# Performance work log

Measured on AMD Instinct MI355X. Metric: run time of the kernel, lower is better.

Reference implementation:

```python
import jax, jax.numpy as jnp
import numpy as np

B, S, E, H, F = 8, 1024, 1024, 16, 4096
D = E // H  # head_dim = 64
EPS = 1e-5


def setup_inputs() -> dict:
    key = jax.random.key(0)
    ks = jax.random.split(key, 12)
    s = 0.02
    return {
        "x": jax.random.normal(ks[0], (B, S, E), dtype=jnp.float32),
        # per-head projections (shared across heads), torch stores [out,in]; we use [in,out]
        "Wq": jax.random.normal(ks[1], (D, D), dtype=jnp.float32) * s,
        "Wk": jax.random.normal(ks[2], (D, D), dtype=jnp.float32) * s,
        "Wv": jax.random.normal(ks[3], (D, D), dtype=jnp.float32) * s,
        "Wo": jax.random.normal(ks[4], (E, E), dtype=jnp.float32) * s,
        "bo": jnp.zeros((E,), dtype=jnp.float32),
        "W1": jax.random.normal(ks[5], (E, F), dtype=jnp.float32) * s,
        "b1": jnp.zeros((F,), dtype=jnp.float32),
        "W2": jax.random.normal(ks[6], (F, E), dtype=jnp.float32) * s,
        "b2": jnp.zeros((E,), dtype=jnp.float32),
        "g1": jnp.ones((E,), dtype=jnp.float32),
        "beta1": jnp.zeros((E,), dtype=jnp.float32),
        "g2": jnp.ones((E,), dtype=jnp.float32),
        "beta2": jnp.zeros((E,), dtype=jnp.float32),
    }


def _layer_norm(x, g, b):
    m = jnp.mean(x, axis=-1, keepdims=True)
    v = jnp.mean(jnp.square(x - m), axis=-1, keepdims=True)
    return (x - m) * jax.lax.rsqrt(v + EPS) * g + b


def reference(x, Wq, Wk, Wv, Wo, bo, W1, b1, W2, b2, g1, beta1, g2, beta2):
    b, s, e = x.shape
    # --- attention sublayer (pre-norm) ---
    nx = _layer_norm(x, g1, beta1)
    h = nx.reshape(b, s, H, D)              # [B,S,H,D]
    q = h @ Wq                               # per-head linear, weight shared over heads
    k = h @ Wk
    v = h @ Wv
    energy = jnp.einsum('bqhd,bkhd->bhqk', q, k)  # full [B,H,S,S] scores
    mask = jnp.tril(jnp.ones((s, s), dtype=bool))
    energy = jnp.where(mask, energy, -jnp.inf)
    att = jax.nn.softmax(energy / jnp.sqrt(jnp.float32(e)), axis=-1)  # NOTE: scale by sqrt(embed_dim)
    o = jnp.einsum('bhqk,bkhd->bqhd', att, v).reshape(b, s, e)
    x = x + (o @ Wo + bo)
    # --- MLP sublayer (pre-norm); dropout is identity in eval ---
    nx = _layer_norm(x, g2, beta2)
    x = x + (jax.nn.relu(nx @ W1 + b1) @ W2 + b2)
    return x
```

## Files before the change

kernel.cpp:

```cpp
#include <hip/hip_runtime.h>

typedef unsigned short u16;
typedef __attribute__((ext_vector_type(4))) float f4;
typedef __attribute__((ext_vector_type(8))) short s8v;
typedef __attribute__((ext_vector_type(4))) unsigned short u16x4;

#define DEVINL __device__ __forceinline__

DEVINL float b2f(u16 u) { union { unsigned i; float f; } x; x.i = ((unsigned)u) << 16; return x.f; }
DEVINL u16 f2b(float f) {
  union { float f; unsigned i; } x; x.f = f;
  unsigned r = 0x7FFFu + ((x.i >> 16) & 1u);
  return (u16)((x.i + r) >> 16);
}

#define GLD_LDS16(g, l)                                                        \
  __builtin_amdgcn_global_load_lds((__attribute__((address_space(1))) void*)(g), \
                                   (__attribute__((address_space(3))) void*)(l), 16, 0, 0)

__global__ __launch_bounds__(256) void k_transpose(const float* __restrict__ in,
                                                   u16* __restrict__ out, int R, int C) {
  __shared__ float t[32][33];
  int tx = threadIdx.x & 31, ty = threadIdx.x >> 5;
  int c0 = blockIdx.x * 32, r0 = blockIdx.y * 32;
#pragma unroll
  for (int i = 0; i < 32; i += 8)
    t[ty + i][tx] = in[(long)(r0 + ty + i) * C + (c0 + tx)];
  __syncthreads();
#pragma unroll
  for (int i = 0; i < 32; i += 8)
    out[(long)(c0 + ty + i) * R + (r0 + tx)] = f2b(t[tx][ty + i]);
}

__global__ __launch_bounds__(256) void k_vtrans(const u16* __restrict__ v, u16* __restrict__ vt) {
  __shared__ u16 t[64][72];
  int bh = blockIdx.x, b = bh >> 4, h = bh & 15;
  int s0 = blockIdx.y * 64;
  int tid = threadIdx.x;
#pragma unroll
  for (int p = 0; p < 2; ++p) {
    int idx = p * 256 + tid;
    int sl = idx >> 3, c8 = (idx & 7) * 8;
    *(s8v*)(&t[sl][c8]) = *(const s8v*)(v + (((long)(b * 1024 + s0 + sl) * 16 + h) * 64) + c8);
  }
  __syncthreads();
#pragma unroll
  for (int p = 0; p < 2; ++p) {
    int idx = p * 256 + tid;
    int d = idx >> 3, c8 = (idx & 7) * 8;
    s8v o;
#pragma unroll
    for (int e = 0; e < 8; ++e) o[e] = (short)t[c8 + e][d];
    *(s8v*)(vt + ((long)bh * 64 + d) * 1024 + s0 + c8) = o;
  }
}

__global__ __launch_bounds__(256) void k_layernorm(const float* __restrict__ x,
                                                   const float* __restrict__ g,
                                                   const float* __restrict__ be,
                                                   u16* __restrict__ out) {
  long row = blockIdx.x;
  int tid = threadIdx.x;
  f4 v = ((const f4*)(x + row * 1024))[tid];
  float s = v[0] + v[1] + v[2] + v[3];
  float s2 = v[0] * v[0] + v[1] * v[1] + v[2] * v[2] + v[3] * v[3];
#pragma unroll
  for (int off = 32; off > 0; off >>= 1) {
    s += __shfl_down(s, off, 64);
    s2 += __shfl_down(s2, off, 64);
  }
  __shared__ float red[8];
  int wv = tid >> 6, ln = tid & 63;
  if (ln == 0) { red[wv] = s; red[4 + wv] = s2; }
  __syncthreads();
  s = red[0] + red[1] + red[2] + red[3];
  s2 = red[4] + red[5] + red[6] + red[7];
  float mean = s * (1.0f / 1024.0f);
  float var = s2 * (1.0f / 1024.0f) - mean * mean;
  float rs = rsqrtf(var + 1e-5f);
  f4 gg = ((const f4*)g)[tid];
  f4 bb = ((const f4*)be)[tid];
  u16x4 o;
#pragma unroll
  for (int i = 0; i < 4; ++i) o[i] = f2b((v[i] - mean) * rs * gg[i] + bb[i]);
  ((u16x4*)(out + row * 1024))[tid] = o;
}

__global__ __launch_bounds__(256) void k_qkv(const u16* __restrict__ nx, const u16* __restrict__ WqT,
                                             const u16* __restrict__ WkT, const u16* __restrict__ WvT,
                                             u16* __restrict__ q, u16* __restrict__ k,
                                             u16* __restrict__ v) {
  int tid = threadIdx.x, lane = tid & 63, wave = tid >> 6;
  int quad = lane >> 4, l16 = lane & 15;
  long rbase = (long)blockIdx.x * 64 + wave * 16;
  s8v a0 = *(const s8v*)(nx + (rbase + l16) * 64 + quad * 8);
  s8v a1 = *(const s8v*)(nx + (rbase + l16) * 64 + 32 + quad * 8);
  const u16* Ws[3] = {WqT, WkT, WvT};
  u16* Os[3] = {q, k, v};
#pragma unroll
  for (int t = 0; t < 3; ++t) {
#pragma unroll
    for (int j = 0; j < 4; ++j) {
      s8v b0 = *(const s8v*)(Ws[t] + (j * 16 + l16) * 64 + quad * 8);
      s8v b1 = *(const s8v*)(Ws[t] + (j * 16 + l16) * 64 + 32 + quad * 8);
      f4 acc = {0.f, 0.f, 0.f, 0.f};
      acc = __builtin_amdgcn_mfma_f32_16x16x32_bf16(a0, b0, acc, 0, 0, 0);
      acc = __builtin_amdgcn_mfma_f32_16x16x32_bf16(a1, b1, acc, 0, 0, 0);
#pragma unroll
      for (int r = 0; r < 4; ++r)
        Os[t][(rbase + quad * 4 + r) * 64 + j * 16 + l16] = f2b(acc[r]);
    }
  }
}

__global__ __launch_bounds__(256) void k_attn_mfma(const u16* __restrict__ q,
                                                   const u16* __restrict__ kk,
                                                   const u16* __restrict__ vt,
                                                   u16* __restrict__ o) {
  constexpr int LDK = 72;
  __shared__ u16 Ks[64 * LDK];
  __shared__ u16 Vt[64 * LDK];
  __shared__ u16 Ps[4][16 * LDK];
  int tid = threadIdx.x, lane = tid & 63, wave = tid >> 6;
  int quad = lane >> 4, l16 = lane & 15;
  int b = blockIdx.x >> 4, h = blockIdx.x & 15;
  int qi = (int)gridDim.y - 1 - (int)blockIdx.y;
  int q0 = qi * 64 + wave * 16;

  const u16* qp = q + (((long)(b * 1024 + q0 + l16)) * 16 + h) * 64;
  s8v aq0 = *(const s8v*)(qp + quad * 8);
  s8v aq1 = *(const s8v*)(qp + 32 + quad * 8);

  f4 O[4];
  float m_[4], l_[4];
#pragma unroll
  for (int jd = 0; jd < 4; ++jd) O[jd] = f4{0.f, 0.f, 0.f, 0.f};
#pragma unroll
  for (int r = 0; r < 4; ++r) { m_[r] = -__builtin_inff(); l_[r] = 0.f; }

  for (int kt = 0; kt <= qi; ++kt) {
    __syncthreads();
#pragma unroll
    for (int p = 0; p < 2; ++p) {
      int idx = p * 256 + tid;
      int row = idx >> 3, c8 = (idx & 7) * 8;
      *(s8v*)(Ks + row * LDK + c8) =
          *(const s8v*)(kk + (((long)(b * 1024 + kt * 64 + row)) * 16 + h) * 64 + c8);
      *(s8v*)(Vt + row * LDK + c8) =
          *(const s8v*)(vt + ((long)blockIdx.x * 64 + row) * 1024 + kt * 64 + c8);
    }
    __syncthreads();

    f4 sf[4];
#pragma unroll
    for (int jn = 0; jn < 4; ++jn) {
      s8v b0 = *(const s8v*)(Ks + (jn * 16 + l16) * LDK + quad * 8);
      s8v b1 = *(const s8v*)(Ks + (jn * 16 + l16) * LDK + 32 + quad * 8);
      f4 acc = f4{0.f, 0.f, 0.f, 0.f};
      acc = __builtin_amdgcn_mfma_f32_16x16x32_bf16(aq0, b0, acc, 0, 0, 0);
      acc = __builtin_amdgcn_mfma_f32_16x16x32_bf16(aq1, b1, acc, 0, 0, 0);
      sf[jn] = acc;
    }
    bool diag = (kt == qi);
    float rm[4];
#pragma unroll
    for (int r = 0; r < 4; ++r) rm[r] = -__builtin_inff();
#pragma unroll
    for (int jn = 0; jn < 4; ++jn)
#pragma unroll
      for (int r = 0; r < 4; ++r) {
        float v = sf[jn][r] * 0.03125f;
        if (diag && (jn * 16 + l16 > wave * 16 + quad * 4 + r)) v = -__builtin_inff();
        sf[jn][r] = v;
        rm[r] = fmaxf(rm[r], v);
      }
#pragma unroll
    for (int off = 1; off < 16; off <<= 1)
#pragma unroll
      for (int r = 0; r < 4; ++r) rm[r] = fmaxf(rm[r], __shfl_xor(rm[r], off, 64));
    float alpha[4], rs[4];
#pragma unroll
    for (int r = 0; r < 4; ++r) {
      float mn = fmaxf(m_[r], rm[r]);
      alpha[r] = __expf(m_[r] - mn);
      m_[r] = mn;
      rs[r] = 0.f;
    }
#pragma unroll
    for (int jn = 0; jn < 4; ++jn)
#pragma unroll
      for (int r = 0; r < 4; ++r) {
        float p = __expf(sf[jn][r] - m_[r]);
        rs[r] += p;
        Ps[wave][(quad * 4 + r) * LDK + jn * 16 + l16] = f2b(p);
      }
#pragma unroll
    for (int off = 1; off < 16; off <<= 1)
#pragma unroll
      for (int r = 0; r < 4; ++r) rs[r] += __shfl_xor(rs[r], off, 64);
#pragma unroll
    for (int r = 0; r < 4; ++r) l_[r] = l_[r] * alpha[r] + rs[r];
#pragma unroll
    for (int jd = 0; jd < 4; ++jd)
#pragma unroll
      for (int r = 0; r < 4; ++r) O[jd][r] *= alpha[r];
    asm volatile("s_waitcnt lgkmcnt(0)" ::: "memory");
    s8v p0 = *(const s8v*)(&Ps[wave][l16 * LDK + quad * 8]);
    s8v p1 = *(const s8v*)(&Ps[wave][l16 * LDK + 32 + quad * 8]);
#pragma unroll
    for (int jd = 0; jd < 4; ++jd) {
      s8v b0 = *(const s8v*)(Vt + (jd * 16 + l16) * LDK + quad * 8);
      s8v b1 = *(const s8v*)(Vt + (jd * 16 + l16) * LDK + 32 + quad * 8);
      O[jd] = __builtin_amdgcn_mfma_f32_16x16x32_bf16(p0, b0, O[jd], 0, 0, 0);
      O[jd] = __builtin_amdgcn_mfma_f32_16x16x32_bf16(p1, b1, O[jd], 0, 0, 0);
    }
  }
#pragma unroll
  for (int r = 0; r < 4; ++r) {
    float inv = 1.0f / l_[r];
    u16* op = o + (((long)(b * 1024 + q0 + quad * 4 + r)) * 16 + h) * 64;
#pragma unroll
    for (int jd = 0; jd < 4; ++jd) op[jd * 16 + l16] = f2b(O[jd][r] * inv);
  }
}

template <int EPI>
__global__ __launch_bounds__(256) void k_gemm_bt(const u16* __restrict__ A, const u16* __restrict__ BT,
                                                 const float* __restrict__ bias,
                                                 const float* __restrict__ resid,
                                                 void* __restrict__ outp, int M, int N, int K) {
  __shared__ u16 sA[3][128 * 32];
  __shared__ u16 sB[3][128 * 32];
  int tid = threadIdx.x, lane = tid & 63, wave = tid >> 6;
  int quad = lane >> 4, l16 = lane & 15;
  int wm = wave >> 1, wn = wave & 1;
  long bm = blockIdx.x, bn = blockIdx.y;
  int srow = tid >> 2, scol = (tid & 3) * 8;
  const u16* ga = A + (bm * 128 + srow) * (long)K + scol;
  const u16* gb = BT + (bn * 128 + srow) * (long)K + scol;
  int woff = wave * 1024;

  f4 acc[4][4];
#pragma unroll
  for (int i = 0; i < 4; ++i)
#pragma unroll
    for (int j = 0; j < 4; ++j) acc[i][j] = f4{0.f, 0.f, 0.f, 0.f};

#pragma unroll
  for (int t = 0; t < 2; ++t) {
    char* lA = (char*)&sA[t][0] + woff;
    char* lB = (char*)&sB[t][0] + woff;
    GLD_LDS16(ga + t * 32, lA);
    GLD_LDS16(ga + 64 * (long)K + t * 32, lA + 4096);
    GLD_LDS16(gb + t * 32, lB);
    GLD_LDS16(gb + 64 * (long)K + t * 32, lB + 4096);
  }

  int cur = 0;
  for (int k0 = 0; k0 < K; k0 += 32) {
    int k2 = k0 + 64;
    if (k2 < K) {
      asm volatile("s_waitcnt vmcnt(4)\n\ts_barrier" ::: "memory");
      int nb = cur >= 1 ? cur - 1 : 2;
      char* lA = (char*)&sA[nb][0] + woff;
      char* lB = (char*)&sB[nb][0] + woff;
      GLD_LDS16(ga + k2, lA);
      GLD_LDS16(ga + 64 * (long)K + k2, lA + 4096);
      GLD_LDS16(gb + k2, lB);
      GLD_LDS16(gb + 64 * (long)K + k2, lB + 4096);
    } else {
      asm volatile("s_waitcnt vmcnt(0)\n\ts_barrier" ::: "memory");
    }
    const u16* cA = sA[cur];
    const u16* cB = sB[cur];
    s8v aF[4], bF[4];
#pragma unroll
    for (int i = 0; i < 4; ++i)
      aF[i] = *(const s8v*)(cA + (wm * 64 + i * 16 + l16) * 32 + quad * 8);
#pragma unroll
    for (int j = 0; j < 4; ++j)
      bF[j] = *(const s8v*)(cB + (wn * 64 + j * 16 + l16) * 32 + quad * 8);
#pragma unroll
    for (int i = 0; i < 4; ++i)
#pragma unroll
      for (int j = 0; j < 4; ++j)
        acc[i][j] = __builtin_amdgcn_mfma_f32_16x16x32_bf16(aF[i], bF[j], acc[i][j], 0, 0, 0);
    cur = cur < 2 ? cur + 1 : 0;
  }

#pragma unroll
  for (int i = 0; i < 4; ++i) {
#pragma unroll
    for (int j = 0; j < 4; ++j) {
      long row = bm * 128 + wm * 64 + i * 16 + quad * 4;
      int col = (int)bn * 128 + wn * 64 + j * 16 + l16;
      float bcol = bias[col];
#pragma unroll
      for (int r = 0; r < 4; ++r) {
        float val = acc[i][j][r] + bcol;
        if (EPI == 1) {
          ((u16*)outp)[(row + r) * (long)N + col] = f2b(val > 0.f ? val : 0.f);
        } else {
          ((float*)outp)[(row + r) * (long)N + col] = resid[(row + r) * (long)N + col] + val;
        }
      }
    }
  }
}

extern "C" void kernel_launch(void* const* d_in, const int* in_sizes, int n_in, void* d_out,
                              int out_size, void* d_ws, size_t ws_size, hipStream_t stream) {
  const float* x = (const float*)d_in[0];
  const float* Wq = (const float*)d_in[1];
  const float* Wk = (const float*)d_in[2];
  const float* Wv = (const float*)d_in[3];
  const float* Wo = (const float*)d_in[4];
  const float* bo = (const float*)d_in[5];
  const float* W1 = (const float*)d_in[6];
  const float* b1 = (const float*)d_in[7];
  const float* W2 = (const float*)d_in[8];
  const float* b2 = (const float*)d_in[9];
  const float* g1 = (const float*)d_in[10];
  const float* be1 = (const float*)d_in[11];
  const float* g2 = (const float*)d_in[12];
  const float* be2 = (const float*)d_in[13];

  char* ws = (char*)d_ws;
  const size_t MB = 1ull << 20;
  u16* nx = (u16*)(ws + 0);
  u16* qb = (u16*)(ws + 16 * MB);
  u16* kb = (u16*)(ws + 32 * MB);
  u16* vb = (u16*)(ws + 48 * MB);
  float* x1 = (float*)(ws + 64 * MB);
  u16* h1 = (u16*)(ws + 96 * MB);
  u16* vtr = (u16*)(ws + 96 * MB);
  u16* WoT = (u16*)(ws + 160 * MB);
  u16* W1T = (u16*)(ws + 162 * MB);
  u16* W2T = (u16*)(ws + 170 * MB);
  u16* WqT = (u16*)(ws + 178 * MB);
  u16* WkT = WqT + 64 * 64;
  u16* WvT = WkT + 64 * 64;
  u16* ob = nx;
  u16* nx2 = qb;

  k_transpose<<<dim3(32, 32), 256, 0, stream>>>(Wo, WoT, 1024, 1024);
  k_transpose<<<dim3(128, 32), 256, 0, stream>>>(W1, W1T, 1024, 4096);
  k_transpose<<<dim3(32, 128), 256, 0, stream>>>(W2, W2T, 4096, 1024);
  k_transpose<<<dim3(2, 2), 256, 0, stream>>>(Wq, WqT, 64, 64);
  k_transpose<<<dim3(2, 2), 256, 0, stream>>>(Wk, WkT, 64, 64);
  k_transpose<<<dim3(2, 2), 256, 0, stream>>>(Wv, WvT, 64, 64);

  k_layernorm<<<8192, 256, 0, stream>>>(x, g1, be1, nx);
  k_qkv<<<2048, 256, 0, stream>>>(nx, WqT, WkT, WvT, qb, kb, vb);
  k_vtrans<<<dim3(128, 16), 256, 0, stream>>>(vb, vtr);
  k_attn_mfma<<<dim3(128, 16), 256, 0, stream>>>(qb, kb, vtr, ob);
  k_gemm_bt<2><<<dim3(64, 8), 256, 0, stream>>>(ob, WoT, bo, x, x1, 8192, 1024, 1024);

  k_layernorm<<<8192, 256, 0, stream>>>(x1, g2, be2, nx2);
  k_gemm_bt<1><<<dim3(64, 32), 256, 0, stream>>>(nx2, W1T, b1, nullptr, h1, 8192, 4096, 1024);
  k_gemm_bt<2><<<dim3(64, 8), 256, 0, stream>>>(h1, W2T, b2, x1, d_out, 8192, 1024, 4096);
}
```

Before: 457.0 us.

## Enlarge attention query tile, fold softmax scale into Q, store residual as bf16

```diff
diff --git a/kernel.cpp b/kernel.cpp
--- a/kernel.cpp
+++ b/kernel.cpp
@@ -55,13 +55,20 @@
   }
 }
 
-__global__ __launch_bounds__(256) void k_layernorm(const float* __restrict__ x,
+template <int IT>
+__global__ __launch_bounds__(256) void k_layernorm(const void* __restrict__ xv,
                                                    const float* __restrict__ g,
                                                    const float* __restrict__ be,
                                                    u16* __restrict__ out) {
   long row = blockIdx.x;
   int tid = threadIdx.x;
-  f4 v = ((const f4*)(x + row * 1024))[tid];
+  f4 v;
+  if (IT == 0) {
+    v = ((const f4*)((const float*)xv + row * 1024))[tid];
+  } else {
+    u16x4 t = ((const u16x4*)((const u16*)xv + row * 1024))[tid];
+    v = f4{b2f(t[0]), b2f(t[1]), b2f(t[2]), b2f(t[3])};
+  }
   float s = v[0] + v[1] + v[2] + v[3];
   float s2 = v[0] * v[0] + v[1] * v[1] + v[2] * v[2] + v[3] * v[3];
 #pragma unroll
@@ -99,6 +106,7 @@
   u16* Os[3] = {q, k, v};
 #pragma unroll
   for (int t = 0; t < 3; ++t) {
+    const float scale = (t == 0) ? 0.03125f : 1.0f;
 #pragma unroll
     for (int j = 0; j < 4; ++j) {
       s8v b0 = *(const s8v*)(Ws[t] + (j * 16 + l16) * 64 + quad * 8);
@@ -108,7 +116,7 @@
       acc = __builtin_amdgcn_mfma_f32_16x16x32_bf16(a1, b1, acc, 0, 0, 0);
 #pragma unroll
       for (int r = 0; r < 4; ++r)
-        Os[t][(rbase + quad * 4 + r) * 64 + j * 16 + l16] = f2b(acc[r]);
+        Os[t][(rbase + quad * 4 + r) * 64 + j * 16 + l16] = f2b(acc[r] * scale);
     }
   }
 }
@@ -120,25 +128,35 @@
   constexpr int LDK = 72;
   __shared__ u16 Ks[64 * LDK];
   __shared__ u16 Vt[64 * LDK];
-  __shared__ u16 Ps[4][16 * LDK];
+  __shared__ u16 Ps[4][32 * LDK];
   int tid = threadIdx.x, lane = tid & 63, wave = tid >> 6;
   int quad = lane >> 4, l16 = lane & 15;
   int b = blockIdx.x >> 4, h = blockIdx.x & 15;
   int qi = (int)gridDim.y - 1 - (int)blockIdx.y;
-  int q0 = qi * 64 + wave * 16;
-
-  const u16* qp = q + (((long)(b * 1024 + q0 + l16)) * 16 + h) * 64;
-  s8v aq0 = *(const s8v*)(qp + quad * 8);
-  s8v aq1 = *(const s8v*)(qp + 32 + quad * 8);
-
-  f4 O[4];
-  float m_[4], l_[4];
-#pragma unroll
-  for (int jd = 0; jd < 4; ++jd) O[jd] = f4{0.f, 0.f, 0.f, 0.f};
-#pragma unroll
-  for (int r = 0; r < 4; ++r) { m_[r] = -__builtin_inff(); l_[r] = 0.f; }
-
-  for (int kt = 0; kt <= qi; ++kt) {
+  int Q0 = qi * 128;
+  int q0 = Q0 + wave * 32;
+
+  s8v aq[2][2];
+#pragma unroll
+  for (int mt = 0; mt < 2; ++mt) {
+    const u16* qp = q + (((long)(b * 1024 + q0 + mt * 16 + l16)) * 16 + h) * 64;
+    aq[mt][0] = *(const s8v*)(qp + quad * 8);
+    aq[mt][1] = *(const s8v*)(qp + 32 + quad * 8);
+  }
+
+  f4 O[2][4];
+  float m_[2][4], l_[2][4];
+#pragma unroll
+  for (int mt = 0; mt < 2; ++mt)
+#pragma unroll
+    for (int jd = 0; jd < 4; ++jd) O[mt][jd] = f4{0.f, 0.f, 0.f, 0.f};
+#pragma unroll
+  for (int mt = 0; mt < 2; ++mt)
+#pragma unroll
+    for (int r = 0; r < 4; ++r) { m_[mt][r] = -__builtin_inff(); l_[mt][r] = 0.f; }
+
+  int ntiles = 2 * qi + 2;
+  for (int kt = 0; kt < ntiles; ++kt) {
     __syncthreads();
 #pragma unroll
     for (int p = 0; p < 2; ++p) {
@@ -151,83 +169,96 @@
     }
     __syncthreads();
 
-    f4 sf[4];
-#pragma unroll
-    for (int jn = 0; jn < 4; ++jn) {
-      s8v b0 = *(const s8v*)(Ks + (jn * 16 + l16) * LDK + quad * 8);
-      s8v b1 = *(const s8v*)(Ks + (jn * 16 + l16) * LDK + 32 + quad * 8);
-      f4 acc = f4{0.f, 0.f, 0.f, 0.f};
-      acc = __builtin_amdgcn_mfma_f32_16x16x32_bf16(aq0, b0, acc, 0, 0, 0);
-      acc = __builtin_amdgcn_mfma_f32_16x16x32_bf16(aq1, b1, acc, 0, 0, 0);
-      sf[jn] = acc;
-    }
-    bool diag = (kt == qi);
-    float rm[4];
-#pragma unroll
-    for (int r = 0; r < 4; ++r) rm[r] = -__builtin_inff();
-#pragma unroll
-    for (int jn = 0; jn < 4; ++jn)
+    bool pv[2];
+#pragma unroll
+    for (int mt = 0; mt < 2; ++mt) {
+      int base = q0 + mt * 16;
+      pv[mt] = (kt * 64 <= base + 15);
+      if (!pv[mt]) continue;
+      f4 sf[4];
+#pragma unroll
+      for (int jn = 0; jn < 4; ++jn) {
+        s8v b0 = *(const s8v*)(Ks + (jn * 16 + l16) * LDK + quad * 8);
+        s8v b1 = *(const s8v*)(Ks + (jn * 16 + l16) * LDK + 32 + quad * 8);
+        f4 acc = f4{0.f, 0.f, 0.f, 0.f};
+        acc = __builtin_amdgcn_mfma_f32_16x16x32_bf16(aq[mt][0], b0, acc, 0, 0, 0);
+        acc = __builtin_amdgcn_mfma_f32_16x16x32_bf16(aq[mt][1], b1, acc, 0, 0, 0);
+        sf[jn] = acc;
+      }
+      bool diag = (kt * 64 + 63 > base);
+      float rm[4];
+#pragma unroll
+      for (int r = 0; r < 4; ++r) rm[r] = -__builtin_inff();
+#pragma unroll
+      for (int jn = 0; jn < 4; ++jn)
+#pragma unroll
+        for (int r = 0; r < 4; ++r) {
+          float v = sf[jn][r];
+          if (diag && (kt * 64 + jn * 16 + l16 > base + quad * 4 + r)) v = -__builtin_inff();
+          sf[jn][r] = v;
+          rm[r] = fmaxf(rm[r], v);
+        }
+#pragma unroll
+      for (int off = 1; off < 16; off <<= 1)
+#pragma unroll
+        for (int r = 0; r < 4; ++r) rm[r] = fmaxf(rm[r], __shfl_xor(rm[r], off, 64));
+      float alpha[4], rs[4];
 #pragma unroll
       for (int r = 0; r < 4; ++r) {
-        float v = sf[jn][r] * 0.03125f;
-        if (diag && (jn * 16 + l16 > wave * 16 + quad * 4 + r)) v = -__builtin_inff();
-        sf[jn][r] = v;
-        rm[r] = fmaxf(rm[r], v);
+        float mn = fmaxf(m_[mt][r], rm[r]);
+        alpha[r] = __expf(m_[mt][r] - mn);
+        m_[mt][r] = mn;
+        rs[r] = 0.f;
       }
 #pragma unroll
-    for (int off = 1; off < 16; off <<= 1)
-#pragma unroll
-      for (int r = 0; r < 4; ++r) rm[r] = fmaxf(rm[r], __shfl_xor(rm[r], off, 64));
-    float alpha[4], rs[4];
+      for (int jn = 0; jn < 4; ++jn)
+#pragma unroll
+        for (int r = 0; r < 4; ++r) {
+          float p = __expf(sf[jn][r] - m_[mt][r]);
+          rs[r] += p;
+          Ps[wave][(mt * 16 + quad * 4 + r) * LDK + jn * 16 + l16] = f2b(p);
+        }
+#pragma unroll
+      for (int off = 1; off < 16; off <<= 1)
+#pragma unroll
+        for (int r = 0; r < 4; ++r) rs[r] += __shfl_xor(rs[r], off, 64);
+#pragma unroll
+      for (int r = 0; r < 4; ++r) l_[mt][r] = l_[mt][r] * alpha[r] + rs[r];
+#pragma unroll
+      for (int jd = 0; jd < 4; ++jd)
+#pragma unroll
+        for (int r = 0; r < 4; ++r) O[mt][jd][r] *= alpha[r];
+    }
+    asm volatile("s_waitcnt lgkmcnt(0)" ::: "memory");
+#pragma unroll
+    for (int jd = 0; jd < 4; ++jd) {
+      s8v vb0 = *(const s8v*)(Vt + (jd * 16 + l16) * LDK + quad * 8);
+      s8v vb1 = *(const s8v*)(Vt + (jd * 16 + l16) * LDK + 32 + quad * 8);
+#pragma unroll
+      for (int mt = 0; mt < 2; ++mt) {
+        if (!pv[mt]) continue;
+        s8v p0 = *(const s8v*)(&Ps[wave][(mt * 16 + l16) * LDK + quad * 8]);
+        s8v p1 = *(const s8v*)(&Ps[wave][(mt * 16 + l16) * LDK + 32 + quad * 8]);
+        O[mt][jd] = __builtin_amdgcn_mfma_f32_16x16x32_bf16(p0, vb0, O[mt][jd], 0, 0, 0);
+        O[mt][jd] = __builtin_amdgcn_mfma_f32_16x16x32_bf16(p1, vb1, O[mt][jd], 0, 0, 0);
+      }
+    }
+  }
+#pragma unroll
+  for (int mt = 0; mt < 2; ++mt)
 #pragma unroll
     for (int r = 0; r < 4; ++r) {
-      float mn = fmaxf(m_[r], rm[r]);
-      alpha[r] = __expf(m_[r] - mn);
-      m_[r] = mn;
-      rs[r] = 0.f;
-    }
-#pragma unroll
-    for (int jn = 0; jn < 4; ++jn)
-#pragma unroll
-      for (int r = 0; r < 4; ++r) {
-        float p = __expf(sf[jn][r] - m_[r]);
-        rs[r] += p;
-        Ps[wave][(quad * 4 + r) * LDK + jn * 16 + l16] = f2b(p);
-      }
-#pragma unroll
-    for (int off = 1; off < 16; off <<= 1)
-#pragma unroll
-      for (int r = 0; r < 4; ++r) rs[r] += __shfl_xor(rs[r], off, 64);
-#pragma unroll
-    for (int r = 0; r < 4; ++r) l_[r] = l_[r] * alpha[r] + rs[r];
-#pragma unroll
-    for (int jd = 0; jd < 4; ++jd)
-#pragma unroll
-      for (int r = 0; r < 4; ++r) O[jd][r] *= alpha[r];
-    asm volatile("s_waitcnt lgkmcnt(0)" ::: "memory");
-    s8v p0 = *(const s8v*)(&Ps[wave][l16 * LDK + quad * 8]);
-    s8v p1 = *(const s8v*)(&Ps[wave][l16 * LDK + 32 + quad * 8]);
-#pragma unroll
-    for (int jd = 0; jd < 4; ++jd) {
-      s8v b0 = *(const s8v*)(Vt + (jd * 16 + l16) * LDK + quad * 8);
-      s8v b1 = *(const s8v*)(Vt + (jd * 16 + l16) * LDK + 32 + quad * 8);
-      O[jd] = __builtin_amdgcn_mfma_f32_16x16x32_bf16(p0, b0, O[jd], 0, 0, 0);
-      O[jd] = __builtin_amdgcn_mfma_f32_16x16x32_bf16(p1, b1, O[jd], 0, 0, 0);
-    }
-  }
-#pragma unroll
-  for (int r = 0; r < 4; ++r) {
-    float inv = 1.0f / l_[r];
-    u16* op = o + (((long)(b * 1024 + q0 + quad * 4 + r)) * 16 + h) * 64;
-#pragma unroll
-    for (int jd = 0; jd < 4; ++jd) op[jd * 16 + l16] = f2b(O[jd][r] * inv);
-  }
+      float inv = 1.0f / l_[mt][r];
+      u16* op = o + (((long)(b * 1024 + q0 + mt * 16 + quad * 4 + r)) * 16 + h) * 64;
+#pragma unroll
+      for (int jd = 0; jd < 4; ++jd) op[jd * 16 + l16] = f2b(O[mt][jd][r] * inv);
+    }
 }
 
 template <int EPI>
 __global__ __launch_bounds__(256) void k_gemm_bt(const u16* __restrict__ A, const u16* __restrict__ BT,
                                                  const float* __restrict__ bias,
-                                                 const float* __restrict__ resid,
+                                                 const void* __restrict__ residv,
                                                  void* __restrict__ outp, int M, int N, int K) {
   __shared__ u16 sA[3][128 * 32];
   __shared__ u16 sB[3][128 * 32];
@@ -298,10 +329,14 @@
 #pragma unroll
       for (int r = 0; r < 4; ++r) {
         float val = acc[i][j][r] + bcol;
+        long idx = (row + r) * (long)N + col;
         if (EPI == 1) {
-          ((u16*)outp)[(row + r) * (long)N + col] = f2b(val > 0.f ? val : 0.f);
+          ((u16*)outp)[idx] = f2b(val > 0.f ? val : 0.f);
         } else {
-          ((float*)outp)[(row + r) * (long)N + col] = resid[(row + r) * (long)N + col] + val;
+          float rv = (EPI == 4) ? b2f(((const u16*)residv)[idx]) : ((const float*)residv)[idx];
+          float o = rv + val;
+          if (EPI == 3) ((u16*)outp)[idx] = f2b(o);
+          else ((float*)outp)[idx] = o;
         }
       }
     }
@@ -331,7 +366,7 @@
   u16* qb = (u16*)(ws + 16 * MB);
   u16* kb = (u16*)(ws + 32 * MB);
   u16* vb = (u16*)(ws + 48 * MB);
-  float* x1 = (float*)(ws + 64 * MB);
+  u16* x1b = (u16*)(ws + 64 * MB);
   u16* h1 = (u16*)(ws + 96 * MB);
   u16* vtr = (u16*)(ws + 96 * MB);
   u16* WoT = (u16*)(ws + 160 * MB);
@@ -350,13 +385,13 @@
   k_transpose<<<dim3(2, 2), 256, 0, stream>>>(Wk, WkT, 64, 64);
   k_transpose<<<dim3(2, 2), 256, 0, stream>>>(Wv, WvT, 64, 64);
 
-  k_layernorm<<<8192, 256, 0, stream>>>(x, g1, be1, nx);
+  k_layernorm<0><<<8192, 256, 0, stream>>>(x, g1, be1, nx);
   k_qkv<<<2048, 256, 0, stream>>>(nx, WqT, WkT, WvT, qb, kb, vb);
   k_vtrans<<<dim3(128, 16), 256, 0, stream>>>(vb, vtr);
-  k_attn_mfma<<<dim3(128, 16), 256, 0, stream>>>(qb, kb, vtr, ob);
-  k_gemm_bt<2><<<dim3(64, 8), 256, 0, stream>>>(ob, WoT, bo, x, x1, 8192, 1024, 1024);
-
-  k_layernorm<<<8192, 256, 0, stream>>>(x1, g2, be2, nx2);
+  k_attn_mfma<<<dim3(128, 8), 256, 0, stream>>>(qb, kb, vtr, ob);
+  k_gemm_bt<3><<<dim3(64, 8), 256, 0, stream>>>(ob, WoT, bo, x, x1b, 8192, 1024, 1024);
+
+  k_layernorm<1><<<8192, 256, 0, stream>>>(x1b, g2, be2, nx2);
   k_gemm_bt<1><<<dim3(64, 32), 256, 0, stream>>>(nx2, W1T, b1, nullptr, h1, 8192, 4096, 1024);
-  k_gemm_bt<2><<<dim3(64, 8), 256, 0, stream>>>(h1, W2T, b2, x1, d_out, 8192, 1024, 4096);
-}
+  k_gemm_bt<4><<<dim3(64, 8), 256, 0, stream>>>(h1, W2T, b2, x1b, d_out, 8192, 1024, 4096);
+}
```

Result: no change. 465.4 us (+1.8%).
